# Optimization experiments

Measured on AMD Instinct MI355X. Metric: run time of the kernel, lower is better.

The kernel has to match this reference:

```python
import jax, jax.numpy as jnp
import numpy as np

H = 6      # n_attention_heads
BLK = 64


def adder1x1(x2d, w):
    """AdderNet 1x1 'convolution': Y[co, n] = -sum_ci |x2d[ci, n] - w[co, ci]|.
    Processed in output-channel blocks to bound the abs-diff intermediate.
    x2d: [Ci, N], w: [Co, Ci] -> [Co, N]
    """
    co, ci = w.shape
    wb = w.reshape(co // BLK, BLK, ci)
    def f(wblk):  # wblk: [BLK, Ci] -> [BLK, N]
        return -jnp.sum(jnp.abs(x2d[None, :, :] - wblk[:, :, None]), axis=1)
    return jax.lax.map(f, wb).reshape(co, -1)


def layernorm_all(y, w, b, eps=1e-5):
    # nn.LayerNorm([E, B, S]) applied to [1, E, B, S]: normalize over ALL of E,B,S
    mu = jnp.mean(y)
    var = jnp.mean((y - mu) ** 2)
    return (y - mu) * jax.lax.rsqrt(var + eps) * w + b


def layernorm_last(y, w, b, eps=1e-5):
    mu = jnp.mean(y, axis=-1, keepdims=True)
    var = jnp.mean((y - mu) ** 2, axis=-1, keepdims=True)
    return (y - mu) * jax.lax.rsqrt(var + eps) * w + b


def setup_inputs() -> dict:
    key = jax.random.key(0)
    ks = jax.random.split(key, 14)
    B, S, E = 8, 197, 384
    inp = {
        "x": jax.random.normal(ks[0], (B, S, E), jnp.float32),
        "wq": jax.random.normal(ks[1], (E, E), jnp.float32) * 0.05,
        "wk": jax.random.normal(ks[2], (E, E), jnp.float32) * 0.05,
        "wv": jax.random.normal(ks[3], (E, E), jnp.float32) * 0.05,
        "qln_w": 1.0 + 0.02 * jax.random.normal(ks[4], (E, B, S), jnp.float32),
        "qln_b": 0.02 * jax.random.normal(ks[5], (E, B, S), jnp.float32),
        "kln_w": 1.0 + 0.02 * jax.random.normal(ks[6], (E, B, S), jnp.float32),
        "kln_b": 0.02 * jax.random.normal(ks[7], (E, B, S), jnp.float32),
        "vln_w": 1.0 + 0.02 * jax.random.normal(ks[8], (E, B, S), jnp.float32),
        "vln_b": 0.02 * jax.random.normal(ks[9], (E, B, S), jnp.float32),
        "oln_w": 1.0 + 0.02 * jax.random.normal(ks[10], (E,), jnp.float32),
        "oln_b": 0.02 * jax.random.normal(ks[11], (E,), jnp.float32),
        "fc_w": jax.random.normal(ks[12], (E, E), jnp.float32) * 0.05,
        "fc_b": 0.02 * jax.random.normal(ks[13], (E,), jnp.float32),
    }
    return inp


def reference(x, wq, wk, wv, qln_w, qln_b, kln_w, kln_b, vln_w, vln_b,
              oln_w, oln_b, fc_w, fc_b):
    B, S, E = x.shape
    D = E // H
    scale = (2.0 * D * (1.0 - 2.0 / np.pi)) ** (-0.5)

    # torch: x.reshape(1, E, B, S) on contiguous [B,S,E] is a flat-buffer reshape
    x2d = x.reshape(E, B * S)  # [Ci, N]

    def proj(w, lw, lb):
        y = adder1x1(x2d, w).reshape(E, B, S)          # adder2d 1x1, bias=False
        y = layernorm_all(y, lw, lb)                    # LN over [E,B,S]
        y = y.reshape(B, S, H, D)                       # flat reshape (as torch)
        y = jnp.swapaxes(y, 1, 2)                       # [B,H,S,D]
        return y.reshape(B * H, S, D)

    q = proj(wq, qln_w, qln_b)
    k = proj(wk, kln_w, kln_b)
    v = proj(wv, vln_w, vln_b)

    att = jnp.einsum('bsd,btd->bst', q, k) * scale      # [B*H, S, S]
    att = jax.nn.softmax(att, axis=-1) + jnp.eye(S, dtype=x.dtype)
    o = jnp.einsum('bst,btd->bsd', att, v)              # [B*H, S, D]

    o = jnp.swapaxes(o.reshape(B, H, S, D), 1, 2).reshape(B, S, E)
    o = layernorm_last(o, oln_w, oln_b)
    return o @ fc_w.T + fc_b
```

## Files before the change

kernel.cpp:

```cpp
#include <hip/hip_runtime.h>
#include <math.h>

#ifndef M_PI
#define M_PI 3.14159265358979323846
#endif

#define B_ 8
#define S_ 197
#define E_ 384
#define H_ 6
#define D_ 64
#define N_ (B_*S_)
#define EN ((size_t)E_*N_)
#define ATT_LD 200
#define NBLK_ADD 300

__global__ __launch_bounds__(256) void k_adder(
    const float* __restrict__ x,
    const float* __restrict__ wq, const float* __restrict__ wk,
    const float* __restrict__ wv,
    float* __restrict__ Y, float* __restrict__ partials)
{
  const int p = blockIdx.z;
  const float* __restrict__ w = (p == 0) ? wq : (p == 1) ? wk : wv;
  const int co0 = blockIdx.x * 64;
  const int n0  = blockIdx.y * 32;

  __shared__ float Xs[16][32];
  __shared__ float Ws[16][64];
  __shared__ float red[8];

  const int tid = threadIdx.x;
  const int tx = tid & 15;
  const int ty = tid >> 4;

  const int xr = tid >> 4, xc = (tid & 15) * 2;
  const int wr = tid >> 2, wc = (tid & 3) * 4;

  const bool xok = (n0 + xc + 1) < N_;
  const float* xg = x + (size_t)xr * N_ + n0 + xc;
  const float* wg = w + (size_t)(co0 + wr) * E_ + wc;

  float2 xv = xok ? *(const float2*)xg : make_float2(0.f, 0.f);
  float4 wv4 = *(const float4*)wg;

  float acc[4][2];
  #pragma unroll
  for (int i = 0; i < 4; ++i) { acc[i][0] = 0.f; acc[i][1] = 0.f; }

  #pragma unroll 1
  for (int t = 0; t < 24; ++t) {
    if (t > 0) __syncthreads();
    *(float2*)(&Xs[xr][xc]) = xv;
    Ws[wc + 0][wr] = wv4.x; Ws[wc + 1][wr] = wv4.y;
    Ws[wc + 2][wr] = wv4.z; Ws[wc + 3][wr] = wv4.w;
    __syncthreads();
    if (t < 23) {
      xg += (size_t)16 * N_;
      wg += 16;
      xv = xok ? *(const float2*)xg : make_float2(0.f, 0.f);
      wv4 = *(const float4*)wg;
    }
    #pragma unroll
    for (int cc = 0; cc < 16; ++cc) {
      float2 x2 = *(const float2*)(&Xs[cc][tx * 2]);
      float4 w4 = *(const float4*)(&Ws[cc][ty * 4]);
      float xa[2] = {x2.x, x2.y};
      float wa[4] = {w4.x, w4.y, w4.z, w4.w};
      #pragma unroll
      for (int i = 0; i < 4; ++i)
        #pragma unroll
        for (int j = 0; j < 2; ++j)
          acc[i][j] += fabsf(xa[j] - wa[i]);
    }
  }

  float s1 = 0.f, s2 = 0.f;
  const int nb = n0 + tx * 2;
  if (nb + 1 < N_) {
    #pragma unroll
    for (int i = 0; i < 4; ++i) {
      int co = co0 + ty * 4 + i;
      float2 yv;
      yv.x = -acc[i][0]; yv.y = -acc[i][1];
      *(float2*)(Y + (size_t)p * EN + (size_t)co * N_ + nb) = yv;
      s1 += yv.x + yv.y;
      s2 += yv.x * yv.x + yv.y * yv.y;
    }
  }
  #pragma unroll
  for (int off = 32; off > 0; off >>= 1) {
    s1 += __shfl_down(s1, off);
    s2 += __shfl_down(s2, off);
  }
  int wid = tid >> 6, lane = tid & 63;
  if (lane == 0) { red[wid * 2] = s1; red[wid * 2 + 1] = s2; }
  __syncthreads();
  if (tid == 0) {
    float t1 = red[0] + red[2] + red[4] + red[6];
    float t2 = red[1] + red[3] + red[5] + red[7];
    int blk = blockIdx.x * gridDim.y + blockIdx.y;
    partials[((size_t)p * NBLK_ADD + blk) * 2 + 0] = t1;
    partials[((size_t)p * NBLK_ADD + blk) * 2 + 1] = t2;
  }
}

__global__ __launch_bounds__(256) void k_stats(
    const float* __restrict__ partials, float* __restrict__ stats)
{
  const int p = blockIdx.x;
  const int tid = threadIdx.x;
  float s1 = 0.f, s2 = 0.f;
  for (int i = tid; i < NBLK_ADD; i += 256) {
    s1 += partials[((size_t)p * NBLK_ADD + i) * 2 + 0];
    s2 += partials[((size_t)p * NBLK_ADD + i) * 2 + 1];
  }
  #pragma unroll
  for (int off = 32; off > 0; off >>= 1) {
    s1 += __shfl_down(s1, off);
    s2 += __shfl_down(s2, off);
  }
  __shared__ float red[8];
  int wid = tid >> 6, lane = tid & 63;
  if (lane == 0) { red[wid * 2] = s1; red[wid * 2 + 1] = s2; }
  __syncthreads();
  if (tid == 0) {
    float S1 = red[0] + red[2] + red[4] + red[6];
    float S2 = red[1] + red[3] + red[5] + red[7];
    float mean = S1 / (float)EN;
    float var = S2 / (float)EN - mean * mean;
    stats[p * 2 + 0] = mean;
    stats[p * 2 + 1] = rsqrtf(var + 1e-5f);
  }
}

__global__ __launch_bounds__(256) void k_lnall(
    const float* __restrict__ Y, const float* __restrict__ stats,
    const float* __restrict__ w0, const float* __restrict__ b0,
    const float* __restrict__ w1, const float* __restrict__ b1,
    const float* __restrict__ w2, const float* __restrict__ b2,
    float* __restrict__ Z)
{
  const int p = blockIdx.y;
  const float* __restrict__ w = (p == 0) ? w0 : (p == 1) ? w1 : w2;
  const float* __restrict__ b = (p == 0) ? b0 : (p == 1) ? b1 : b2;
  const float mean = stats[p * 2 + 0];
  const float rstd = stats[p * 2 + 1];
  size_t i = ((size_t)blockIdx.x * 256 + threadIdx.x) * 4;
  const float* Yp = Y + (size_t)p * EN;
  float* Zp = Z + (size_t)p * EN;
  float4 y = *(const float4*)(Yp + i);
  float4 wv = *(const float4*)(w + i);
  float4 bv = *(const float4*)(b + i);
  float4 z;
  z.x = (y.x - mean) * rstd * wv.x + bv.x;
  z.y = (y.y - mean) * rstd * wv.y + bv.y;
  z.z = (y.z - mean) * rstd * wv.z + bv.z;
  z.w = (y.w - mean) * rstd * wv.w + bv.w;
  *(float4*)(Zp + i) = z;
}

__global__ __launch_bounds__(256) void k_qk(
    const float* __restrict__ zq, const float* __restrict__ zk,
    float* __restrict__ att, float scale)
{
  const int bh = blockIdx.x, b = bh / H_, h = bh % H_;
  const int s0 = blockIdx.y * 64, t0 = blockIdx.z * 64;
  __shared__ float Qs[64][68];
  __shared__ float Ks[64][68];
  const int tid = threadIdx.x;
  {
    int rl = tid >> 4, c4 = (tid & 15) * 4;
    for (int rr = rl; rr < 64; rr += 16) {
      int s = s0 + rr;
      float4 v = make_float4(0.f, 0.f, 0.f, 0.f);
      if (s < S_) v = *(const float4*)(zq + (size_t)(b * S_ + s) * E_ + h * D_ + c4);
      Qs[c4 + 0][rr] = v.x; Qs[c4 + 1][rr] = v.y;
      Qs[c4 + 2][rr] = v.z; Qs[c4 + 3][rr] = v.w;
      int t = t0 + rr;
      float4 u = make_float4(0.f, 0.f, 0.f, 0.f);
      if (t < S_) u = *(const float4*)(zk + (size_t)(b * S_ + t) * E_ + h * D_ + c4);
      Ks[c4 + 0][rr] = u.x; Ks[c4 + 1][rr] = u.y;
      Ks[c4 + 2][rr] = u.z; Ks[c4 + 3][rr] = u.w;
    }
  }
  __syncthreads();
  const int r0 = (tid >> 4) * 4, c0 = (tid & 15) * 4;
  float acc[4][4];
  #pragma unroll
  for (int i = 0; i < 4; ++i)
    #pragma unroll
    for (int j = 0; j < 4; ++j) acc[i][j] = 0.f;
  #pragma unroll 8
  for (int d = 0; d < 64; ++d) {
    float4 q4 = *(const float4*)(&Qs[d][r0]);
    float4 k4 = *(const float4*)(&Ks[d][c0]);
    float qa[4] = {q4.x, q4.y, q4.z, q4.w};
    float ka[4] = {k4.x, k4.y, k4.z, k4.w};
    #pragma unroll
    for (int i = 0; i < 4; ++i)
      #pragma unroll
      for (int j = 0; j < 4; ++j)
        acc[i][j] += qa[i] * ka[j];
  }
  #pragma unroll
  for (int i = 0; i < 4; ++i) {
    int s = s0 + r0 + i;
    if (s < S_) {
      #pragma unroll
      for (int j = 0; j < 4; ++j) {
        int t = t0 + c0 + j;
        if (t < S_)
          att[((size_t)bh * S_ + s) * ATT_LD + t] = acc[i][j] * scale;
      }
    }
  }
}

__global__ __launch_bounds__(256) void k_softmax(float* __restrict__ att)
{
  const int row = blockIdx.x * 4 + (threadIdx.x >> 6);
  const int lane = threadIdx.x & 63;
  const int s = row % S_;
  float* base = att + (size_t)row * ATT_LD;
  float v[4];
  float m = -1e30f;
  #pragma unroll
  for (int j = 0; j < 4; ++j) {
    int t = lane + 64 * j;
    v[j] = (t < S_) ? base[t] : -1e30f;
    m = fmaxf(m, v[j]);
  }
  #pragma unroll
  for (int off = 32; off > 0; off >>= 1) m = fmaxf(m, __shfl_xor(m, off));
  float sum = 0.f;
  #pragma unroll
  for (int j = 0; j < 4; ++j) {
    int t = lane + 64 * j;
    v[j] = (t < S_) ? __expf(v[j] - m) : 0.f;
    sum += v[j];
  }
  #pragma unroll
  for (int off = 32; off > 0; off >>= 1) sum += __shfl_xor(sum, off);
  float inv = 1.f / sum;
  #pragma unroll
  for (int j = 0; j < 4; ++j) {
    int t = lane + 64 * j;
    if (t < S_) base[t] = v[j] * inv + ((t == s) ? 1.f : 0.f);
  }
}

__global__ __launch_bounds__(256) void k_pv(
    const float* __restrict__ att, const float* __restrict__ zv,
    float* __restrict__ obuf)
{
  const int bh = blockIdx.x, b = bh / H_, h = bh % H_;
  const int s0 = blockIdx.y * 64;
  __shared__ float As[64][68];
  __shared__ float Vs[64][68];
  const int tid = threadIdx.x;
  const int r0 = (tid >> 4) * 4, d0 = (tid & 15) * 4;
  float acc[4][4];
  #pragma unroll
  for (int i = 0; i < 4; ++i)
    #pragma unroll
    for (int j = 0; j < 4; ++j) acc[i][j] = 0.f;

  for (int tt = 0; tt < 256; tt += 64) {
    {
      int sl = tid >> 4, t4 = (tid & 15) * 4;
      for (int rr = sl; rr < 64; rr += 16) {
        int s = s0 + rr;
        #pragma unroll
        for (int k = 0; k < 4; ++k) {
          int t = tt + t4 + k;
          float a = 0.f;
          if (s < S_ && t < S_) a = att[((size_t)bh * S_ + s) * ATT_LD + t];
          As[t4 + k][rr] = a;
        }
        int t = tt + rr;
        float4 v = make_float4(0.f, 0.f, 0.f, 0.f);
        if (t < S_) v = *(const float4*)(zv + (size_t)(b * S_ + t) * E_ + h * D_ + t4);
        *(float4*)(&Vs[rr][t4]) = v;
      }
    }
    __syncthreads();
    #pragma unroll 8
    for (int t = 0; t < 64; ++t) {
      float4 a4 = *(const float4*)(&As[t][r0]);
      float4 v4 = *(const float4*)(&Vs[t][d0]);
      float aa[4] = {a4.x, a4.y, a4.z, a4.w};
      float va[4] = {v4.x, v4.y, v4.z, v4.w};
      #pragma unroll
      for (int i = 0; i < 4; ++i)
        #pragma unroll
        for (int j = 0; j < 4; ++j)
          acc[i][j] += aa[i] * va[j];
    }
    __syncthreads();
  }
  #pragma unroll
  for (int i = 0; i < 4; ++i) {
    int s = s0 + r0 + i;
    if (s < S_) {
      float4 o = make_float4(acc[i][0], acc[i][1], acc[i][2], acc[i][3]);
      *(float4*)(obuf + (size_t)(b * S_ + s) * E_ + h * D_ + d0) = o;
    }
  }
}

__global__ __launch_bounds__(256) void k_lnlast(
    const float* __restrict__ obuf,
    const float* __restrict__ lw, const float* __restrict__ lb,
    float* __restrict__ oln)
{
  const int row = blockIdx.x * 4 + (threadIdx.x >> 6);
  const int lane = threadIdx.x & 63;
  const float* base = obuf + (size_t)row * E_;
  float v[6];
  float s1 = 0.f;
  #pragma unroll
  for (int j = 0; j < 6; ++j) { v[j] = base[lane + 64 * j]; s1 += v[j]; }
  #pragma unroll
  for (int off = 32; off > 0; off >>= 1) s1 += __shfl_xor(s1, off);
  float mean = s1 * (1.f / E_);
  float s2 = 0.f;
  #pragma unroll
  for (int j = 0; j < 6; ++j) { float d = v[j] - mean; s2 += d * d; }
  #pragma unroll
  for (int off = 32; off > 0; off >>= 1) s2 += __shfl_xor(s2, off);
  float rstd = rsqrtf(s2 * (1.f / E_) + 1e-5f);
  float* ob = oln + (size_t)row * E_;
  #pragma unroll
  for (int j = 0; j < 6; ++j) {
    int e = lane + 64 * j;
    ob[e] = (v[j] - mean) * rstd * lw[e] + lb[e];
  }
}

__global__ __launch_bounds__(256) void k_fc(
    const float* __restrict__ oln, const float* __restrict__ fcw,
    const float* __restrict__ fcb, float* __restrict__ out)
{
  const int j0 = blockIdx.x * 64, n0 = blockIdx.y * 64;
  __shared__ float Xs[16][64];
  __shared__ float Ws[16][64];
  const int tid = threadIdx.x;
  const int tx = tid & 15, ty = tid >> 4;
  float acc[4][4];
  #pragma unroll
  for (int i = 0; i < 4; ++i)
    #pragma unroll
    for (int j = 0; j < 4; ++j) acc[i][j] = 0.f;

  for (int e0 = 0; e0 < E_; e0 += 16) {
    {
      int nl = tid >> 2, c4 = (tid & 3) * 4;
      int n = n0 + nl;
      float4 v = make_float4(0.f, 0.f, 0.f, 0.f);
      if (n < N_) v = *(const float4*)(oln + (size_t)n * E_ + e0 + c4);
      Xs[c4 + 0][nl] = v.x; Xs[c4 + 1][nl] = v.y;
      Xs[c4 + 2][nl] = v.z; Xs[c4 + 3][nl] = v.w;
      float4 u = *(const float4*)(fcw + (size_t)(j0 + nl) * E_ + e0 + c4);
      Ws[c4 + 0][nl] = u.x; Ws[c4 + 1][nl] = u.y;
      Ws[c4 + 2][nl] = u.z; Ws[c4 + 3][nl] = u.w;
    }
    __syncthreads();
    #pragma unroll
    for (int cc = 0; cc < 16; ++cc) {
      float4 xv = *(const float4*)(&Xs[cc][tx * 4]);
      float4 wv4 = *(const float4*)(&Ws[cc][ty * 4]);
      float xa[4] = {xv.x, xv.y, xv.z, xv.w};
      float wa[4] = {wv4.x, wv4.y, wv4.z, wv4.w};
      #pragma unroll
      for (int i = 0; i < 4; ++i)
        #pragma unroll
        for (int j = 0; j < 4; ++j)
          acc[i][j] += wa[i] * xa[j];
    }
    __syncthreads();
  }
  #pragma unroll
  for (int jj = 0; jj < 4; ++jj) {
    int n = n0 + tx * 4 + jj;
    if (n < N_) {
      int jc = j0 + ty * 4;
      float4 o;
      o.x = acc[0][jj] + fcb[jc + 0];
      o.y = acc[1][jj] + fcb[jc + 1];
      o.z = acc[2][jj] + fcb[jc + 2];
      o.w = acc[3][jj] + fcb[jc + 3];
      *(float4*)(out + (size_t)n * E_ + jc) = o;
    }
  }
}

extern "C" void kernel_launch(void* const* d_in, const int* in_sizes, int n_in,
                              void* d_out, int out_size, void* d_ws, size_t ws_size,
                              hipStream_t stream)
{
  const float* x   = (const float*)d_in[0];
  const float* wq  = (const float*)d_in[1];
  const float* wk  = (const float*)d_in[2];
  const float* wv  = (const float*)d_in[3];
  const float* qw  = (const float*)d_in[4];
  const float* qb  = (const float*)d_in[5];
  const float* kw  = (const float*)d_in[6];
  const float* kb  = (const float*)d_in[7];
  const float* vw  = (const float*)d_in[8];
  const float* vb  = (const float*)d_in[9];
  const float* ow  = (const float*)d_in[10];
  const float* obp = (const float*)d_in[11];
  const float* fcw = (const float*)d_in[12];
  const float* fcb = (const float*)d_in[13];
  float* out = (float*)d_out;
  float* ws  = (float*)d_ws;

  float* Y     = ws;
  float* Z     = Y + 3 * EN;
  float* att   = Z + 3 * EN;
  float* obuf  = att + (size_t)48 * S_ * ATT_LD;
  float* oln   = obuf + EN;
  float* part  = oln + EN;
  float* stats = part + 3 * NBLK_ADD * 2;

  const float scale = (float)pow(2.0 * D_ * (1.0 - 2.0 / M_PI), -0.5);

  k_adder<<<dim3(6, 50, 3), 256, 0, stream>>>(x, wq, wk, wv, Y, part);
  k_stats<<<dim3(3), 256, 0, stream>>>(part, stats);
  k_lnall<<<dim3(591, 3), 256, 0, stream>>>(Y, stats, qw, qb, kw, kb, vw, vb, Z);
  const float* zq = Z;
  const float* zk = Z + EN;
  const float* zv = Z + 2 * EN;
  k_qk<<<dim3(48, 4, 4), 256, 0, stream>>>(zq, zk, att, scale);
  k_softmax<<<dim3(2364), 256, 0, stream>>>(att);
  k_pv<<<dim3(48, 4), 256, 0, stream>>>(att, zv, obuf);
  k_lnlast<<<dim3(394), 256, 0, stream>>>(obuf, ow, obp, oln);
  k_fc<<<dim3(6, 25), 256, 0, stream>>>(oln, fcw, fcb, out);
}
```

Baseline: 128.4 us.

## Split adder reduction over input channels and fuse attention into one kernel

```diff
diff --git a/kernel.cpp b/kernel.cpp
--- a/kernel.cpp
+++ b/kernel.cpp
@@ -12,23 +12,23 @@
 #define D_ 64
 #define N_ (B_*S_)
 #define EN ((size_t)E_*N_)
-#define ATT_LD 200
-#define NBLK_ADD 300
+#define NBLK_RED 591
 
 __global__ __launch_bounds__(256) void k_adder(
     const float* __restrict__ x,
     const float* __restrict__ wq, const float* __restrict__ wk,
     const float* __restrict__ wv,
-    float* __restrict__ Y, float* __restrict__ partials)
-{
-  const int p = blockIdx.z;
+    float* __restrict__ P)
+{
+  const int z = blockIdx.z;
+  const int p = z >> 1, c = z & 1;
   const float* __restrict__ w = (p == 0) ? wq : (p == 1) ? wk : wv;
   const int co0 = blockIdx.x * 64;
   const int n0  = blockIdx.y * 32;
+  const int cib = c * 192;
 
   __shared__ float Xs[16][32];
   __shared__ float Ws[16][64];
-  __shared__ float red[8];
 
   const int tid = threadIdx.x;
   const int tx = tid & 15;
@@ -38,8 +38,8 @@
   const int wr = tid >> 2, wc = (tid & 3) * 4;
 
   const bool xok = (n0 + xc + 1) < N_;
-  const float* xg = x + (size_t)xr * N_ + n0 + xc;
-  const float* wg = w + (size_t)(co0 + wr) * E_ + wc;
+  const float* xg = x + (size_t)(cib + xr) * N_ + n0 + xc;
+  const float* wg = w + (size_t)(co0 + wr) * E_ + cib + wc;
 
   float2 xv = xok ? *(const float2*)xg : make_float2(0.f, 0.f);
   float4 wv4 = *(const float4*)wg;
@@ -49,13 +49,13 @@
   for (int i = 0; i < 4; ++i) { acc[i][0] = 0.f; acc[i][1] = 0.f; }
 
   #pragma unroll 1
-  for (int t = 0; t < 24; ++t) {
+  for (int t = 0; t < 12; ++t) {
     if (t > 0) __syncthreads();
     *(float2*)(&Xs[xr][xc]) = xv;
     Ws[wc + 0][wr] = wv4.x; Ws[wc + 1][wr] = wv4.y;
     Ws[wc + 2][wr] = wv4.z; Ws[wc + 3][wr] = wv4.w;
     __syncthreads();
-    if (t < 23) {
+    if (t < 11) {
       xg += (size_t)16 * N_;
       wg += 16;
       xv = xok ? *(const float2*)xg : make_float2(0.f, 0.f);
@@ -75,33 +75,47 @@
     }
   }
 
-  float s1 = 0.f, s2 = 0.f;
   const int nb = n0 + tx * 2;
   if (nb + 1 < N_) {
     #pragma unroll
     for (int i = 0; i < 4; ++i) {
       int co = co0 + ty * 4 + i;
-      float2 yv;
-      yv.x = -acc[i][0]; yv.y = -acc[i][1];
-      *(float2*)(Y + (size_t)p * EN + (size_t)co * N_ + nb) = yv;
-      s1 += yv.x + yv.y;
-      s2 += yv.x * yv.x + yv.y * yv.y;
-    }
-  }
+      float2 yv; yv.x = acc[i][0]; yv.y = acc[i][1];
+      *(float2*)(P + (size_t)z * EN + (size_t)co * N_ + nb) = yv;
+    }
+  }
+}
+
+__global__ __launch_bounds__(256) void k_reduceY(
+    float* __restrict__ wsbuf, float* __restrict__ partials)
+{
+  const int p = blockIdx.y;
+  float* P0 = wsbuf + (size_t)(2 * p) * EN;
+  const float* P1 = wsbuf + (size_t)(2 * p + 1) * EN;
+  const int tid = threadIdx.x;
+  size_t i = ((size_t)blockIdx.x * 256 + tid) * 4;
+  float4 a = *(const float4*)(P0 + i);
+  float4 b = *(const float4*)(P1 + i);
+  float4 y;
+  y.x = -(a.x + b.x); y.y = -(a.y + b.y);
+  y.z = -(a.z + b.z); y.w = -(a.w + b.w);
+  *(float4*)(P0 + i) = y;
+  float s1 = y.x + y.y + y.z + y.w;
+  float s2 = y.x * y.x + y.y * y.y + y.z * y.z + y.w * y.w;
   #pragma unroll
   for (int off = 32; off > 0; off >>= 1) {
     s1 += __shfl_down(s1, off);
     s2 += __shfl_down(s2, off);
   }
+  __shared__ float red[8];
   int wid = tid >> 6, lane = tid & 63;
   if (lane == 0) { red[wid * 2] = s1; red[wid * 2 + 1] = s2; }
   __syncthreads();
   if (tid == 0) {
     float t1 = red[0] + red[2] + red[4] + red[6];
     float t2 = red[1] + red[3] + red[5] + red[7];
-    int blk = blockIdx.x * gridDim.y + blockIdx.y;
-    partials[((size_t)p * NBLK_ADD + blk) * 2 + 0] = t1;
-    partials[((size_t)p * NBLK_ADD + blk) * 2 + 1] = t2;
+    partials[((size_t)p * NBLK_RED + blockIdx.x) * 2 + 0] = t1;
+    partials[((size_t)p * NBLK_RED + blockIdx.x) * 2 + 1] = t2;
   }
 }
 
@@ -111,9 +125,9 @@
   const int p = blockIdx.x;
   const int tid = threadIdx.x;
   float s1 = 0.f, s2 = 0.f;
-  for (int i = tid; i < NBLK_ADD; i += 256) {
-    s1 += partials[((size_t)p * NBLK_ADD + i) * 2 + 0];
-    s2 += partials[((size_t)p * NBLK_ADD + i) * 2 + 1];
+  for (int i = tid; i < NBLK_RED; i += 256) {
+    s1 += partials[((size_t)p * NBLK_RED + i) * 2 + 0];
+    s2 += partials[((size_t)p * NBLK_RED + i) * 2 + 1];
   }
   #pragma unroll
   for (int off = 32; off > 0; off >>= 1) {
@@ -135,11 +149,10 @@
 }
 
 __global__ __launch_bounds__(256) void k_lnall(
-    const float* __restrict__ Y, const float* __restrict__ stats,
+    float* __restrict__ wsbuf, const float* __restrict__ stats,
     const float* __restrict__ w0, const float* __restrict__ b0,
     const float* __restrict__ w1, const float* __restrict__ b1,
-    const float* __restrict__ w2, const float* __restrict__ b2,
-    float* __restrict__ Z)
+    const float* __restrict__ w2, const float* __restrict__ b2)
 {
   const int p = blockIdx.y;
   const float* __restrict__ w = (p == 0) ? w0 : (p == 1) ? w1 : w2;
@@ -147,8 +160,8 @@
   const float mean = stats[p * 2 + 0];
   const float rstd = stats[p * 2 + 1];
   size_t i = ((size_t)blockIdx.x * 256 + threadIdx.x) * 4;
-  const float* Yp = Y + (size_t)p * EN;
-  float* Zp = Z + (size_t)p * EN;
+  const float* Yp = wsbuf + (size_t)(2 * p) * EN;
+  float* Zp = wsbuf + (size_t)(2 * p + 1) * EN;
   float4 y = *(const float4*)(Yp + i);
   float4 wv = *(const float4*)(w + i);
   float4 bv = *(const float4*)(b + i);
@@ -160,151 +173,156 @@
   *(float4*)(Zp + i) = z;
 }
 
-__global__ __launch_bounds__(256) void k_qk(
+__global__ __launch_bounds__(256) void k_attn(
     const float* __restrict__ zq, const float* __restrict__ zk,
-    float* __restrict__ att, float scale)
+    const float* __restrict__ zv, float* __restrict__ obuf, float scale)
 {
   const int bh = blockIdx.x, b = bh / H_, h = bh % H_;
-  const int s0 = blockIdx.y * 64, t0 = blockIdx.z * 64;
-  __shared__ float Qs[64][68];
-  __shared__ float Ks[64][68];
+  const int s0 = blockIdx.y * 32;
+
+  __shared__ float Qs[64][36];
+  __shared__ float KVs[64][68];
+  __shared__ float Ps[32][200];
+  __shared__ float linv[32];
+
   const int tid = threadIdx.x;
-  {
-    int rl = tid >> 4, c4 = (tid & 15) * 4;
-    for (int rr = rl; rr < 64; rr += 16) {
-      int s = s0 + rr;
-      float4 v = make_float4(0.f, 0.f, 0.f, 0.f);
-      if (s < S_) v = *(const float4*)(zq + (size_t)(b * S_ + s) * E_ + h * D_ + c4);
-      Qs[c4 + 0][rr] = v.x; Qs[c4 + 1][rr] = v.y;
-      Qs[c4 + 2][rr] = v.z; Qs[c4 + 3][rr] = v.w;
-      int t = t0 + rr;
+  const int tx = tid & 15, ty = tid >> 4;
+
+  #pragma unroll
+  for (int it = 0; it < 2; ++it) {
+    int idx = tid + it * 256;
+    int sl = idx >> 4, c4 = (idx & 15) * 4;
+    int s = s0 + sl;
+    float4 v = make_float4(0.f, 0.f, 0.f, 0.f);
+    if (s < S_) v = *(const float4*)(zq + (size_t)(b * S_ + s) * E_ + h * D_ + c4);
+    Qs[c4 + 0][sl] = v.x; Qs[c4 + 1][sl] = v.y;
+    Qs[c4 + 2][sl] = v.z; Qs[c4 + 3][sl] = v.w;
+  }
+
+  float accS[4][2][4];
+  #pragma unroll
+  for (int tt = 0; tt < 4; ++tt)
+    #pragma unroll
+    for (int r = 0; r < 2; ++r)
+      #pragma unroll
+      for (int j = 0; j < 4; ++j) accS[tt][r][j] = 0.f;
+
+  #pragma unroll
+  for (int tt = 0; tt < 4; ++tt) {
+    __syncthreads();
+    #pragma unroll
+    for (int it = 0; it < 4; ++it) {
+      int idx = tid + it * 256;
+      int tl = idx >> 4, c4 = (idx & 15) * 4;
+      int t = tt * 64 + tl;
       float4 u = make_float4(0.f, 0.f, 0.f, 0.f);
       if (t < S_) u = *(const float4*)(zk + (size_t)(b * S_ + t) * E_ + h * D_ + c4);
-      Ks[c4 + 0][rr] = u.x; Ks[c4 + 1][rr] = u.y;
-      Ks[c4 + 2][rr] = u.z; Ks[c4 + 3][rr] = u.w;
-    }
-  }
-  __syncthreads();
-  const int r0 = (tid >> 4) * 4, c0 = (tid & 15) * 4;
-  float acc[4][4];
-  #pragma unroll
-  for (int i = 0; i < 4; ++i)
-    #pragma unroll
-    for (int j = 0; j < 4; ++j) acc[i][j] = 0.f;
-  #pragma unroll 8
-  for (int d = 0; d < 64; ++d) {
-    float4 q4 = *(const float4*)(&Qs[d][r0]);
-    float4 k4 = *(const float4*)(&Ks[d][c0]);
-    float qa[4] = {q4.x, q4.y, q4.z, q4.w};
-    float ka[4] = {k4.x, k4.y, k4.z, k4.w};
-    #pragma unroll
-    for (int i = 0; i < 4; ++i)
-      #pragma unroll
-      for (int j = 0; j < 4; ++j)
-        acc[i][j] += qa[i] * ka[j];
-  }
-  #pragma unroll
-  for (int i = 0; i < 4; ++i) {
-    int s = s0 + r0 + i;
-    if (s < S_) {
+      KVs[c4 + 0][tl] = u.x; KVs[c4 + 1][tl] = u.y;
+      KVs[c4 + 2][tl] = u.z; KVs[c4 + 3][tl] = u.w;
+    }
+    __syncthreads();
+    #pragma unroll 8
+    for (int d = 0; d < 64; ++d) {
+      float2 q2 = *(const float2*)(&Qs[d][2 * ty]);
+      float4 k4 = *(const float4*)(&KVs[d][tx * 4]);
+      float ka[4] = {k4.x, k4.y, k4.z, k4.w};
       #pragma unroll
       for (int j = 0; j < 4; ++j) {
-        int t = t0 + c0 + j;
-        if (t < S_)
-          att[((size_t)bh * S_ + s) * ATT_LD + t] = acc[i][j] * scale;
+        accS[tt][0][j] += q2.x * ka[j];
+        accS[tt][1][j] += q2.y * ka[j];
       }
     }
   }
-}
-
-__global__ __launch_bounds__(256) void k_softmax(float* __restrict__ att)
-{
-  const int row = blockIdx.x * 4 + (threadIdx.x >> 6);
-  const int lane = threadIdx.x & 63;
-  const int s = row % S_;
-  float* base = att + (size_t)row * ATT_LD;
-  float v[4];
-  float m = -1e30f;
-  #pragma unroll
-  for (int j = 0; j < 4; ++j) {
-    int t = lane + 64 * j;
-    v[j] = (t < S_) ? base[t] : -1e30f;
-    m = fmaxf(m, v[j]);
-  }
-  #pragma unroll
-  for (int off = 32; off > 0; off >>= 1) m = fmaxf(m, __shfl_xor(m, off));
-  float sum = 0.f;
-  #pragma unroll
-  for (int j = 0; j < 4; ++j) {
-    int t = lane + 64 * j;
-    v[j] = (t < S_) ? __expf(v[j] - m) : 0.f;
-    sum += v[j];
-  }
-  #pragma unroll
-  for (int off = 32; off > 0; off >>= 1) sum += __shfl_xor(sum, off);
-  float inv = 1.f / sum;
-  #pragma unroll
-  for (int j = 0; j < 4; ++j) {
-    int t = lane + 64 * j;
-    if (t < S_) base[t] = v[j] * inv + ((t == s) ? 1.f : 0.f);
-  }
-}
-
-__global__ __launch_bounds__(256) void k_pv(
-    const float* __restrict__ att, const float* __restrict__ zv,
-    float* __restrict__ obuf)
-{
-  const int bh = blockIdx.x, b = bh / H_, h = bh % H_;
-  const int s0 = blockIdx.y * 64;
-  __shared__ float As[64][68];
-  __shared__ float Vs[64][68];
-  const int tid = threadIdx.x;
-  const int r0 = (tid >> 4) * 4, d0 = (tid & 15) * 4;
-  float acc[4][4];
-  #pragma unroll
-  for (int i = 0; i < 4; ++i)
-    #pragma unroll
-    for (int j = 0; j < 4; ++j) acc[i][j] = 0.f;
-
-  for (int tt = 0; tt < 256; tt += 64) {
-    {
-      int sl = tid >> 4, t4 = (tid & 15) * 4;
-      for (int rr = sl; rr < 64; rr += 16) {
-        int s = s0 + rr;
-        #pragma unroll
-        for (int k = 0; k < 4; ++k) {
-          int t = tt + t4 + k;
-          float a = 0.f;
-          if (s < S_ && t < S_) a = att[((size_t)bh * S_ + s) * ATT_LD + t];
-          As[t4 + k][rr] = a;
-        }
-        int t = tt + rr;
-        float4 v = make_float4(0.f, 0.f, 0.f, 0.f);
-        if (t < S_) v = *(const float4*)(zv + (size_t)(b * S_ + t) * E_ + h * D_ + t4);
-        *(float4*)(&Vs[rr][t4]) = v;
-      }
-    }
-    __syncthreads();
+
+  float mr0 = -1e30f, mr1 = -1e30f;
+  #pragma unroll
+  for (int tt = 0; tt < 4; ++tt)
+    #pragma unroll
+    for (int j = 0; j < 4; ++j) {
+      int t = tt * 64 + tx * 4 + j;
+      float v0 = (t < S_) ? accS[tt][0][j] * scale : -1e30f;
+      float v1 = (t < S_) ? accS[tt][1][j] * scale : -1e30f;
+      accS[tt][0][j] = v0; accS[tt][1][j] = v1;
+      mr0 = fmaxf(mr0, v0); mr1 = fmaxf(mr1, v1);
+    }
+  #pragma unroll
+  for (int off = 1; off < 16; off <<= 1) {
+    mr0 = fmaxf(mr0, __shfl_xor(mr0, off));
+    mr1 = fmaxf(mr1, __shfl_xor(mr1, off));
+  }
+  float sr0 = 0.f, sr1 = 0.f;
+  #pragma unroll
+  for (int tt = 0; tt < 4; ++tt)
+    #pragma unroll
+    for (int j = 0; j < 4; ++j) {
+      float p0 = __expf(accS[tt][0][j] - mr0);
+      float p1 = __expf(accS[tt][1][j] - mr1);
+      accS[tt][0][j] = p0; accS[tt][1][j] = p1;
+      sr0 += p0; sr1 += p1;
+    }
+  #pragma unroll
+  for (int off = 1; off < 16; off <<= 1) {
+    sr0 += __shfl_xor(sr0, off);
+    sr1 += __shfl_xor(sr1, off);
+  }
+  if (tx == 0) { linv[2 * ty] = 1.f / sr0; linv[2 * ty + 1] = 1.f / sr1; }
+  #pragma unroll
+  for (int tt = 0; tt < 4; ++tt) {
+    int t4 = tt * 64 + tx * 4;
+    if (t4 < 200) {
+      *(float4*)(&Ps[2 * ty][t4]) =
+          make_float4(accS[tt][0][0], accS[tt][0][1], accS[tt][0][2], accS[tt][0][3]);
+      *(float4*)(&Ps[2 * ty + 1][t4]) =
+          make_float4(accS[tt][1][0], accS[tt][1][1], accS[tt][1][2], accS[tt][1][3]);
+    }
+  }
+
+  float accO[2][4];
+  #pragma unroll
+  for (int r = 0; r < 2; ++r)
+    #pragma unroll
+    for (int j = 0; j < 4; ++j) accO[r][j] = 0.f;
+
+  #pragma unroll
+  for (int tt = 0; tt < 4; ++tt) {
+    __syncthreads();
+    #pragma unroll
+    for (int it = 0; it < 4; ++it) {
+      int idx = tid + it * 256;
+      int tl = idx >> 4, c4 = (idx & 15) * 4;
+      int t = tt * 64 + tl;
+      float4 u = make_float4(0.f, 0.f, 0.f, 0.f);
+      if (t < S_) u = *(const float4*)(zv + (size_t)(b * S_ + t) * E_ + h * D_ + c4);
+      *(float4*)(&KVs[tl][c4]) = u;
+    }
+    __syncthreads();
+    const int tmax = (tt < 3) ? 64 : 8;
     #pragma unroll 8
-    for (int t = 0; t < 64; ++t) {
-      float4 a4 = *(const float4*)(&As[t][r0]);
-      float4 v4 = *(const float4*)(&Vs[t][d0]);
-      float aa[4] = {a4.x, a4.y, a4.z, a4.w};
+    for (int tl = 0; tl < tmax; ++tl) {
+      float p0 = Ps[2 * ty][tt * 64 + tl];
+      float p1 = Ps[2 * ty + 1][tt * 64 + tl];
+      float4 v4 = *(const float4*)(&KVs[tl][tx * 4]);
       float va[4] = {v4.x, v4.y, v4.z, v4.w};
       #pragma unroll
-      for (int i = 0; i < 4; ++i)
-        #pragma unroll
-        for (int j = 0; j < 4; ++j)
-          acc[i][j] += aa[i] * va[j];
-    }
-    __syncthreads();
-  }
-  #pragma unroll
-  for (int i = 0; i < 4; ++i) {
-    int s = s0 + r0 + i;
+      for (int j = 0; j < 4; ++j) {
+        accO[0][j] += p0 * va[j];
+        accO[1][j] += p1 * va[j];
+      }
+    }
+  }
+
+  #pragma unroll
+  for (int r = 0; r < 2; ++r) {
+    int s = s0 + 2 * ty + r;
     if (s < S_) {
-      float4 o = make_float4(acc[i][0], acc[i][1], acc[i][2], acc[i][3]);
-      *(float4*)(obuf + (size_t)(b * S_ + s) * E_ + h * D_ + d0) = o;
+      float inv = linv[2 * ty + r];
+      float4 vs = *(const float4*)(zv + (size_t)(b * S_ + s) * E_ + h * D_ + tx * 4);
+      float4 o;
+      o.x = accO[r][0] * inv + vs.x;
+      o.y = accO[r][1] * inv + vs.y;
+      o.z = accO[r][2] * inv + vs.z;
+      o.w = accO[r][3] * inv + vs.w;
+      *(float4*)(obuf + (size_t)(b * S_ + s) * E_ + h * D_ + tx * 4) = o;
     }
   }
 }
@@ -416,25 +434,21 @@
   float* out = (float*)d_out;
   float* ws  = (float*)d_ws;
 
-  float* Y     = ws;
-  float* Z     = Y + 3 * EN;
-  float* att   = Z + 3 * EN;
-  float* obuf  = att + (size_t)48 * S_ * ATT_LD;
-  float* oln   = obuf + EN;
-  float* part  = oln + EN;
-  float* stats = part + 3 * NBLK_ADD * 2;
+  float* obuf  = ws + 6 * EN;
+  float* oln   = ws + 7 * EN;
+  float* part  = ws + 8 * EN;
+  float* stats = part + 3 * NBLK_RED * 2;
 
   const float scale = (float)pow(2.0 * D_ * (1.0 - 2.0 / M_PI), -0.5);
 
-  k_adder<<<dim3(6, 50, 3), 256, 0, stream>>>(x, wq, wk, wv, Y, part);
+  k_adder<<<dim3(6, 50, 6), 256, 0, stream>>>(x, wq, wk, wv, ws);
+  k_reduceY<<<dim3(NBLK_RED, 3), 256, 0, stream>>>(ws, part);
   k_stats<<<dim3(3), 256, 0, stream>>>(part, stats);
-  k_lnall<<<dim3(591, 3), 256, 0, stream>>>(Y, stats, qw, qb, kw, kb, vw, vb, Z);
-  const float* zq = Z;
-  const float* zk = Z + EN;
-  const float* zv = Z + 2 * EN;
-  k_qk<<<dim3(48, 4, 4), 256, 0, stream>>>(zq, zk, att, scale);
-  k_softmax<<<dim3(2364), 256, 0, stream>>>(att);
-  k_pv<<<dim3(48, 4), 256, 0, stream>>>(att, zv, obuf);
+  k_lnall<<<dim3(NBLK_RED, 3), 256, 0, stream>>>(ws, stats, qw, qb, kw, kb, vw, vb);
+  const float* zq = ws + 1 * EN;
+  const float* zk = ws + 3 * EN;
+  const float* zv = ws + 5 * EN;
+  k_attn<<<dim3(48, 7), 256, 0, stream>>>(zq, zk, zv, obuf, scale);
   k_lnlast<<<dim3(394), 256, 0, stream>>>(obuf, ow, obp, oln);
   k_fc<<<dim3(6, 25), 256, 0, stream>>>(oln, fcw, fcb, out);
 }
```

After: 114.6 us. 10.8% less time.
